# Kernel optimization log

Hardware: AMD Instinct MI355X
Metric: run time of the kernel (lower is better)

The kernel has to match this reference:

```python
import jax, jax.numpy as jnp
import numpy as np

HEADS = 4
HID = 64
EPS = 1e-5
SLOPE = 0.01  # torch default leaky_relu negative slope


def _lrelu(v):
    return jnp.where(v > 0, v, SLOPE * v)


def _gat_layer(x, e, att, num_nodes):
    # x: [N, H, d], e: [2, E], att: [1, H, 2d]
    d = x.shape[-1]
    att_l = att[0, :, :d]   # [H, d] multiplies src features
    att_r = att[0, :, d:]   # [H, d] multiplies dst features
    # mean over 2d of lrelu(cat(x[e0], x[e1]) * att) decomposes exactly into
    # per-node partial sums (leaky_relu is elementwise), avoiding the [E,H,2d] cat.
    s_l = _lrelu(x * att_l).sum(-1)  # [N, H]
    s_r = _lrelu(x * att_r).sum(-1)  # [N, H]
    s = jnp.exp((s_l[e[0]] + s_r[e[1]]) / (2 * d))  # [E, H]
    msg = x[e[1]] * s[..., None]                    # [E, H, d]
    num = jax.ops.segment_sum(msg, e[0], num_segments=num_nodes)  # [N, H, d]
    den = jax.ops.segment_sum(s, e[0], num_segments=num_nodes)    # [N, H]
    return num / den[..., None]


def _layernorm(h, gamma, beta):
    mu = h.mean(-1, keepdims=True)
    var = ((h - mu) ** 2).mean(-1, keepdims=True)
    return (h - mu) / jnp.sqrt(var + EPS) * gamma + beta


def setup_inputs() -> dict:
    key = jax.random.key(0)
    ks = jax.random.split(key, 10)
    N, DIN, E = 50000, 128, 800000
    H, D = HEADS, HID
    x = jax.random.normal(ks[0], (N, DIN), dtype=jnp.float32)
    edge_index = jax.random.randint(ks[1], (2, E), 0, N, dtype=jnp.int64)
    sc0 = 1.0 / np.sqrt(DIN)
    sc1 = 1.0 / np.sqrt(H * D)
    W0 = jax.random.uniform(ks[2], (H * D, DIN), jnp.float32, -sc0, sc0)
    b0 = jax.random.uniform(ks[3], (H * D,), jnp.float32, -sc0, sc0)
    W1 = jax.random.uniform(ks[4], (H * D, H * D), jnp.float32, -sc1, sc1)
    b1 = jax.random.uniform(ks[5], (H * D,), jnp.float32, -sc1, sc1)
    att0 = jax.random.uniform(ks[6], (1, H, 2 * D), jnp.float32)
    att1 = jax.random.uniform(ks[7], (1, H, 2 * D), jnp.float32)
    gamma = jnp.ones((H * D,), jnp.float32)
    beta = jnp.zeros((H * D,), jnp.float32)
    return {"x": x, "edge_index": edge_index, "W0": W0, "b0": b0,
            "W1": W1, "b1": b1, "att0": att0, "att1": att1,
            "gamma": gamma, "beta": beta}


def reference(x, edge_index, W0, b0, W1, b1, att0, att1, gamma, beta):
    N = x.shape[0]
    H, D = HEADS, HID
    e = edge_index
    # layer 0: gnn Linear -> attention aggregate -> LayerNorm + LeakyReLU
    h0 = (x @ W0.T + b0).reshape(N, H, D)
    a0 = _gat_layer(h0, e, att0, N).reshape(N, H * D)
    x1 = _lrelu(_layernorm(a0, gamma, beta))
    # layer 1 (last): attention aggregate then mean over heads, Identity act
    h1 = (x1 @ W1.T + b1).reshape(N, H, D)
    a1 = _gat_layer(h1, e, att1, N)  # [N, H, D]
    return a1.mean(axis=1)           # [N, D]
```

## Files before the change

kernel.cpp:

```cpp
#include <hip/hip_runtime.h>
#include <hip/hip_bf16.h>
#include <type_traits>

#define NN 50000
#define EE 800000
#define HH 4
#define DD 64
#define HD 256
#define DIN 128

typedef short bf16x8 __attribute__((ext_vector_type(8)));
typedef float f32x4 __attribute__((ext_vector_type(4)));

__device__ inline ushort f2bf(float x) {
    __hip_bfloat16 b = __float2bfloat16(x);
    return __builtin_bit_cast(ushort, b);
}
__device__ inline float bf2f(ushort u) {
    return __uint_as_float((uint)u << 16);
}

__device__ inline void gload16(const ushort* src, ushort* lds_dst) {
    __builtin_amdgcn_global_load_lds(
        (const __attribute__((address_space(1))) void*)src,
        (__attribute__((address_space(3))) void*)lds_dst, 16, 0, 0);
}


__global__ void hist_kernel(const int* __restrict__ e0, int* __restrict__ cnt, int E) {
    int i = blockIdx.x * 256 + threadIdx.x;
    if (i < E) atomicAdd(&cnt[e0[i]], 1);
}

__global__ __launch_bounds__(1024) void scanA_kernel(const int* __restrict__ cnt,
                                                     int* __restrict__ incl,
                                                     int* __restrict__ tot, int N) {
    __shared__ int buf[2][1024];
    int b = blockIdx.x, t = threadIdx.x;
    int i = b * 1024 + t;
    int v = (i < N) ? cnt[i] : 0;
    buf[0][t] = v;
    __syncthreads();
    int sel = 0;
    for (int off = 1; off < 1024; off <<= 1) {
        int nv = buf[sel][t];
        if (t >= off) nv += buf[sel][t - off];
        buf[sel ^ 1][t] = nv;
        __syncthreads();
        sel ^= 1;
    }
    if (i < N) incl[i] = buf[sel][t];
    if (t == 1023) tot[b] = buf[sel][1023];
}

__global__ void scanB_kernel(int* __restrict__ tot, int nb) {
    if (threadIdx.x == 0) {
        int s = 0;
        for (int b = 0; b < nb; ++b) {
            int v = tot[b];
            tot[b] = s;
            s += v;
        }
    }
}

__global__ void scanC_kernel(const int* __restrict__ incl, const int* __restrict__ tot,
                             const int* __restrict__ cnt, int* __restrict__ rp,
                             int* __restrict__ cur, int N) {
    int i = blockIdx.x * 256 + threadIdx.x;
    if (i == 0) rp[0] = 0;
    if (i < N) {
        int e = incl[i] + tot[i >> 10];
        rp[i + 1] = e;
        cur[i] = e - cnt[i];
    }
}

__global__ void scatter_kernel(const int* __restrict__ e0, const int* __restrict__ e1,
                               int* __restrict__ cur, int* __restrict__ col, int E) {
    int i = blockIdx.x * 256 + threadIdx.x;
    if (i < E) {
        int pos = atomicAdd(&cur[e0[i]], 1);
        col[pos] = e1[i];
    }
}


__global__ void split_kernel(const float* __restrict__ src, ushort* __restrict__ hi,
                             ushort* __restrict__ lo, int n4) {
    int i = blockIdx.x * 256 + threadIdx.x;
    if (i < n4) {
        float4 v = ((const float4*)src)[i];
        ushort4 h, l;
        h.x = f2bf(v.x); l.x = f2bf(v.x - bf2f(h.x));
        h.y = f2bf(v.y); l.y = f2bf(v.y - bf2f(h.y));
        h.z = f2bf(v.z); l.z = f2bf(v.z - bf2f(h.z));
        h.w = f2bf(v.w); l.w = f2bf(v.w - bf2f(h.w));
        ((ushort4*)hi)[i] = h;
        ((ushort4*)lo)[i] = l;
    }
}


template <int K>
__global__ __launch_bounds__(256) void gemm_mfma(const ushort* __restrict__ Ah,
                                                 const ushort* __restrict__ Al,
                                                 const ushort* __restrict__ Bh,
                                                 const ushort* __restrict__ Bl,
                                                 const float* __restrict__ bias,
                                                 const float* __restrict__ att,
                                                 ushort* __restrict__ Y,
                                                 float* __restrict__ bw,
                                                 int Nrows) {
    __shared__ ushort sh[2][20480];

    const int t = threadIdx.x;
    const int w = t >> 6, lane = t & 63;
    const int lg = lane >> 4;
    const int lm = lane & 15;
    const int row0 = blockIdx.x * 64;

    f32x4 acc[16];
#pragma unroll
    for (int n = 0; n < 16; ++n) acc[n] = (f32x4){0.f, 0.f, 0.f, 0.f};

    auto STAGE = [&](int b, int ks) {
        const int k0 = ks * 32;
        ushort* base = sh[b];
        gload16(Ah + (size_t)(row0 + lane) * K + k0 + w * 8, base + w * 512);
        gload16(Al + (size_t)(row0 + lane) * K + k0 + w * 8, base + 2048 + w * 512);
#pragma unroll
        for (int j2 = 0; j2 < 4; ++j2) {
            gload16(Bh + (size_t)(j2 * 64 + lane) * K + k0 + w * 8,
                    base + 4096 + w * 2048 + j2 * 512);
            gload16(Bl + (size_t)(j2 * 64 + lane) * K + k0 + w * 8,
                    base + 12288 + w * 2048 + j2 * 512);
        }
    };
    auto COMPUTE = [&](int b) {
        ushort* base = sh[b];
        bf16x8 ah = *(const bf16x8*)(base + lg * 512 + (w * 16 + lm) * 8);
        bf16x8 al = *(const bf16x8*)(base + 2048 + lg * 512 + (w * 16 + lm) * 8);
#pragma unroll
        for (int n = 0; n < 16; ++n) {
            bf16x8 bh = *(const bf16x8*)(base + 4096 + lg * 2048 + (n * 16 + lm) * 8);
            bf16x8 bl = *(const bf16x8*)(base + 12288 + lg * 2048 + (n * 16 + lm) * 8);
            acc[n] = __builtin_amdgcn_mfma_f32_16x16x32_bf16(ah, bh, acc[n], 0, 0, 0);
            acc[n] = __builtin_amdgcn_mfma_f32_16x16x32_bf16(ah, bl, acc[n], 0, 0, 0);
            acc[n] = __builtin_amdgcn_mfma_f32_16x16x32_bf16(al, bh, acc[n], 0, 0, 0);
        }
    };

    constexpr int NT = K / 32;
    STAGE(0, 0);
    asm volatile("s_waitcnt vmcnt(0)" ::: "memory");
    __syncthreads();
    int cur = 0;
#pragma unroll
    for (int ks = 0; ks < NT - 1; ++ks) {
        STAGE(cur ^ 1, ks + 1);
        COMPUTE(cur);
        asm volatile("s_waitcnt vmcnt(0)" ::: "memory");
        __syncthreads();
        cur ^= 1;
    }
    COMPUTE(cur);

    const int rbase = row0 + w * 16 + lg * 4;
    float attr[16];
#pragma unroll
    for (int n = 0; n < 16; ++n)
        attr[n] = att[(n >> 2) * 128 + 64 + (n & 3) * 16 + lm];
#pragma unroll
    for (int n = 0; n < 16; ++n) {
        const float bv = bias[n * 16 + lm];
        acc[n][0] += bv; acc[n][1] += bv; acc[n][2] += bv; acc[n][3] += bv;
    }
#pragma unroll
    for (int n = 0; n < 16; ++n) {
        const int c = n * 16 + lm;
#pragma unroll
        for (int r = 0; r < 4; ++r) {
            const int rr = rbase + r;
            if (rr < Nrows) Y[(size_t)rr * HD + c] = f2bf(acc[n][r]);
        }
    }
#pragma unroll
    for (int r = 0; r < 4; ++r) {
        float s0 = 0.f, s1 = 0.f, s2 = 0.f, s3 = 0.f;
#pragma unroll
        for (int n = 0; n < 16; ++n) {
            float p = acc[n][r] * attr[n];
            p = p > 0.f ? p : 0.01f * p;
            if ((n >> 2) == 0) s0 += p;
            else if ((n >> 2) == 1) s1 += p;
            else if ((n >> 2) == 2) s2 += p;
            else s3 += p;
        }
#pragma unroll
        for (int mm = 1; mm < 16; mm <<= 1) {
            s0 += __shfl_xor(s0, mm);
            s1 += __shfl_xor(s1, mm);
            s2 += __shfl_xor(s2, mm);
            s3 += __shfl_xor(s3, mm);
        }
        const int rr = rbase + r;
        if (lm < 4 && rr < Nrows) {
            float sv = lm == 0 ? s0 : lm == 1 ? s1 : lm == 2 ? s2 : s3;
            bw[rr * 4 + lm] = __expf(sv * 0.0078125f);
        }
    }
}


template <bool FINAL>
__global__ __launch_bounds__(256) void gather_kernel(const ushort* __restrict__ hbuf,
                                                     const int* __restrict__ rp,
                                                     const int* __restrict__ col,
                                                     const float* __restrict__ bw,
                                                     const float* __restrict__ gamma,
                                                     const float* __restrict__ beta,
                                                     float* __restrict__ out,
                                                     ushort* __restrict__ ohi,
                                                     ushort* __restrict__ olo) {
    const int t = threadIdx.x;
    const int w = t >> 6;
    const int lane = t & 63;
    const int hh = lane >> 4;
    const int n = blockIdx.x * 4 + w;

    __shared__ int cb[4][64];
    __shared__ float sv[4][256];

    const int start = rp[n], end = rp[n + 1];

    float acc0 = 0.f, acc1 = 0.f, acc2 = 0.f, acc3 = 0.f;
    float dn0 = 0.f, dn1 = 0.f, dn2 = 0.f, dn3 = 0.f;

    for (int base = start; base < end; base += 64) {
        int m = end - base;
        if (m > 64) m = 64;
        if (lane < m) {
            int src = col[base + lane];
            cb[w][lane] = src;
            float4 b4 = *(const float4*)(bw + src * 4);
            dn0 += b4.x; dn1 += b4.y; dn2 += b4.z; dn3 += b4.w;
            *(float4*)&sv[w][lane * 4] = b4;
        }
        __builtin_amdgcn_wave_barrier();
#pragma unroll 8
        for (int j = 0; j < m; ++j) {
            int src = cb[w][j];
            float s = sv[w][j * 4 + hh];
            ushort4 u = *(const ushort4*)(hbuf + (size_t)src * HD + lane * 4);
            acc0 = fmaf(bf2f(u.x), s, acc0);
            acc1 = fmaf(bf2f(u.y), s, acc1);
            acc2 = fmaf(bf2f(u.z), s, acc2);
            acc3 = fmaf(bf2f(u.w), s, acc3);
        }
        __builtin_amdgcn_wave_barrier();
    }

#pragma unroll
    for (int m2 = 32; m2 > 0; m2 >>= 1) {
        dn0 += __shfl_xor(dn0, m2);
        dn1 += __shfl_xor(dn1, m2);
        dn2 += __shfl_xor(dn2, m2);
        dn3 += __shfl_xor(dn3, m2);
    }
    float den = hh == 0 ? dn0 : hh == 1 ? dn1 : hh == 2 ? dn2 : dn3;
    float inv = 1.f / den;
    float r0 = acc0 * inv, r1 = acc1 * inv, r2 = acc2 * inv, r3 = acc3 * inv;

    if (!FINAL) {
        float s = r0 + r1 + r2 + r3;
#pragma unroll
        for (int m2 = 32; m2 > 0; m2 >>= 1) s += __shfl_xor(s, m2);
        float mu = s * (1.f / 256.f);
        float d0 = r0 - mu, d1 = r1 - mu, d2 = r2 - mu, d3 = r3 - mu;
        float vs = d0 * d0 + d1 * d1 + d2 * d2 + d3 * d3;
#pragma unroll
        for (int m2 = 32; m2 > 0; m2 >>= 1) vs += __shfl_xor(vs, m2);
        float rs = rsqrtf(vs * (1.f / 256.f) + 1e-5f);
        float4 g = *(const float4*)(gamma + lane * 4);
        float4 bb = *(const float4*)(beta + lane * 4);
        float y0 = d0 * rs * g.x + bb.x;
        float y1 = d1 * rs * g.y + bb.y;
        float y2 = d2 * rs * g.z + bb.z;
        float y3 = d3 * rs * g.w + bb.w;
        y0 = y0 > 0.f ? y0 : 0.01f * y0;
        y1 = y1 > 0.f ? y1 : 0.01f * y1;
        y2 = y2 > 0.f ? y2 : 0.01f * y2;
        y3 = y3 > 0.f ? y3 : 0.01f * y3;
        ushort4 h, l;
        h.x = f2bf(y0); l.x = f2bf(y0 - bf2f(h.x));
        h.y = f2bf(y1); l.y = f2bf(y1 - bf2f(h.y));
        h.z = f2bf(y2); l.z = f2bf(y2 - bf2f(h.z));
        h.w = f2bf(y3); l.w = f2bf(y3 - bf2f(h.w));
        *(ushort4*)(ohi + (size_t)n * HD + lane * 4) = h;
        *(ushort4*)(olo + (size_t)n * HD + lane * 4) = l;
    } else {
        r0 += __shfl_xor(r0, 16); r0 += __shfl_xor(r0, 32);
        r1 += __shfl_xor(r1, 16); r1 += __shfl_xor(r1, 32);
        r2 += __shfl_xor(r2, 16); r2 += __shfl_xor(r2, 32);
        r3 += __shfl_xor(r3, 16); r3 += __shfl_xor(r3, 32);
        if (lane < 16) {
            *(float4*)(out + (size_t)n * DD + lane * 4) =
                make_float4(r0 * 0.25f, r1 * 0.25f, r2 * 0.25f, r3 * 0.25f);
        }
    }
}


extern "C" void kernel_launch(void* const* d_in, const int* in_sizes, int n_in,
                              void* d_out, int out_size, void* d_ws, size_t ws_size,
                              hipStream_t stream) {
    const float* x     = (const float*)d_in[0];
    const int*   ei    = (const int*)d_in[1];
    const float* W0    = (const float*)d_in[2];
    const float* b0    = (const float*)d_in[3];
    const float* W1    = (const float*)d_in[4];
    const float* b1    = (const float*)d_in[5];
    const float* att0  = (const float*)d_in[6];
    const float* att1  = (const float*)d_in[7];
    const float* gamma = (const float*)d_in[8];
    const float* beta  = (const float*)d_in[9];
    float* out = (float*)d_out;

    const int N = NN, E = EE;

    ushort* ahi = (ushort*)d_ws;
    ushort* alo = ahi + (size_t)N * HD;
    ushort* hb0 = alo + (size_t)N * HD;
    ushort* hb1 = hb0 + (size_t)N * HD;
    ushort* xh  = hb1;
    ushort* xl  = hb1 + (size_t)N * DIN;
    ushort* w0h = hb1 + (size_t)N * HD;
    ushort* w0l = w0h + HD * DIN;
    ushort* w1h = w0l + HD * DIN;
    ushort* w1l = w1h + HD * HD;
    float* bw   = (float*)(w1l + HD * HD);
    int*   cnt  = (int*)(bw + (size_t)N * HH);
    int*   rp   = cnt + N;
    int*   cur  = rp + N + 1;
    int*   col  = cur + N;
    int*   incl = col + E;
    int*   tot  = incl + N;

    const int* e0 = ei;
    const int* e1 = ei + E;

    const int NB = (N + 1023) / 1024;

    hipMemsetAsync(cnt, 0, N * sizeof(int), stream);
    hist_kernel<<<(E + 255) / 256, 256, 0, stream>>>(e0, cnt, E);
    scanA_kernel<<<NB, 1024, 0, stream>>>(cnt, incl, tot, N);
    scanB_kernel<<<1, 64, 0, stream>>>(tot, NB);
    scanC_kernel<<<(N + 255) / 256, 256, 0, stream>>>(incl, tot, cnt, rp, cur, N);
    scatter_kernel<<<(E + 255) / 256, 256, 0, stream>>>(e0, e1, cur, col, E);

    split_kernel<<<(N * DIN / 4 + 255) / 256, 256, 0, stream>>>(x, xh, xl, N * DIN / 4);
    split_kernel<<<(HD * DIN / 4 + 255) / 256, 256, 0, stream>>>(W0, w0h, w0l, HD * DIN / 4);
    split_kernel<<<(HD * HD / 4 + 255) / 256, 256, 0, stream>>>(W1, w1h, w1l, HD * HD / 4);

    const int GB = (N + 63) / 64;

    gemm_mfma<DIN><<<GB, 256, 0, stream>>>(xh, xl, w0h, w0l, b0, att0, hb0, bw, N);
    gather_kernel<false><<<N / 4, 256, 0, stream>>>(hb0, rp, col, bw, gamma, beta,
                                                    nullptr, ahi, alo);

    gemm_mfma<HD><<<GB, 256, 0, stream>>>(ahi, alo, w1h, w1l, b1, att1, hb1, bw, N);
    gather_kernel<true><<<N / 4, 256, 0, stream>>>(hb1, rp, col, bw, gamma, beta,
                                                   out, nullptr, nullptr);
}
```

Measured before the change: 332.3 us.

## Retile GEMM warps over columns, overlap staging with compute, unroll gather loop

Each wave in the MFMA GEMM now owns a 64x64 tile (all 64 rows, one head's 64 columns) instead of 16 rows by 256 columns. This cuts per-step LDS fragment loads from 34 to 16 per wave and lets the attention-score reduction stay inside one wave per head. The pipeline now issues the next stage's loads, then waits with a partial vmcnt so the copy can overlap compute, and uses raw s_barrier instead of syncthreads. The gather inner loop unroll also rises from 8 to 16, which may raise register pressure.

After: 385.5 us. 1.16x slower.

```diff
diff --git a/kernel.cpp b/kernel.cpp
--- a/kernel.cpp
+++ b/kernel.cpp
@@ -120,9 +120,11 @@
     const int lm = lane & 15;
     const int row0 = blockIdx.x * 64;
 
-    f32x4 acc[16];
-#pragma unroll
-    for (int n = 0; n < 16; ++n) acc[n] = (f32x4){0.f, 0.f, 0.f, 0.f};
+    f32x4 acc[4][4];
+#pragma unroll
+    for (int rb = 0; rb < 4; ++rb)
+#pragma unroll
+        for (int cb = 0; cb < 4; ++cb) acc[rb][cb] = (f32x4){0.f, 0.f, 0.f, 0.f};
 
     auto STAGE = [&](int b, int ks) {
         const int k0 = ks * 32;
@@ -139,75 +141,86 @@
     };
     auto COMPUTE = [&](int b) {
         ushort* base = sh[b];
-        bf16x8 ah = *(const bf16x8*)(base + lg * 512 + (w * 16 + lm) * 8);
-        bf16x8 al = *(const bf16x8*)(base + 2048 + lg * 512 + (w * 16 + lm) * 8);
-#pragma unroll
-        for (int n = 0; n < 16; ++n) {
-            bf16x8 bh = *(const bf16x8*)(base + 4096 + lg * 2048 + (n * 16 + lm) * 8);
-            bf16x8 bl = *(const bf16x8*)(base + 12288 + lg * 2048 + (n * 16 + lm) * 8);
-            acc[n] = __builtin_amdgcn_mfma_f32_16x16x32_bf16(ah, bh, acc[n], 0, 0, 0);
-            acc[n] = __builtin_amdgcn_mfma_f32_16x16x32_bf16(ah, bl, acc[n], 0, 0, 0);
-            acc[n] = __builtin_amdgcn_mfma_f32_16x16x32_bf16(al, bh, acc[n], 0, 0, 0);
-        }
+        bf16x8 a_h[4], a_l[4], b_h[4], b_l[4];
+#pragma unroll
+        for (int rb = 0; rb < 4; ++rb) {
+            a_h[rb] = *(const bf16x8*)(base + lg * 512 + (rb * 16 + lm) * 8);
+            a_l[rb] = *(const bf16x8*)(base + 2048 + lg * 512 + (rb * 16 + lm) * 8);
+        }
+#pragma unroll
+        for (int cb = 0; cb < 4; ++cb) {
+            const int c = w * 64 + cb * 16 + lm;
+            b_h[cb] = *(const bf16x8*)(base + 4096 + lg * 2048 + c * 8);
+            b_l[cb] = *(const bf16x8*)(base + 12288 + lg * 2048 + c * 8);
+        }
+#pragma unroll
+        for (int rb = 0; rb < 4; ++rb)
+#pragma unroll
+            for (int cb = 0; cb < 4; ++cb) {
+                acc[rb][cb] = __builtin_amdgcn_mfma_f32_16x16x32_bf16(a_h[rb], b_h[cb],
+                                                                      acc[rb][cb], 0, 0, 0);
+                acc[rb][cb] = __builtin_amdgcn_mfma_f32_16x16x32_bf16(a_h[rb], b_l[cb],
+                                                                      acc[rb][cb], 0, 0, 0);
+                acc[rb][cb] = __builtin_amdgcn_mfma_f32_16x16x32_bf16(a_l[rb], b_h[cb],
+                                                                      acc[rb][cb], 0, 0, 0);
+            }
     };
 
     constexpr int NT = K / 32;
     STAGE(0, 0);
-    asm volatile("s_waitcnt vmcnt(0)" ::: "memory");
-    __syncthreads();
-    int cur = 0;
-#pragma unroll
-    for (int ks = 0; ks < NT - 1; ++ks) {
-        STAGE(cur ^ 1, ks + 1);
-        COMPUTE(cur);
-        asm volatile("s_waitcnt vmcnt(0)" ::: "memory");
-        __syncthreads();
-        cur ^= 1;
-    }
-    COMPUTE(cur);
-
-    const int rbase = row0 + w * 16 + lg * 4;
-    float attr[16];
-#pragma unroll
-    for (int n = 0; n < 16; ++n)
-        attr[n] = att[(n >> 2) * 128 + 64 + (n & 3) * 16 + lm];
-#pragma unroll
-    for (int n = 0; n < 16; ++n) {
-        const float bv = bias[n * 16 + lm];
-        acc[n][0] += bv; acc[n][1] += bv; acc[n][2] += bv; acc[n][3] += bv;
-    }
-#pragma unroll
-    for (int n = 0; n < 16; ++n) {
-        const int c = n * 16 + lm;
+#pragma unroll
+    for (int ks = 0; ks < NT; ++ks) {
+        const int cb_ = ks & 1;
+        if (ks + 1 < NT) {
+            STAGE(cb_ ^ 1, ks + 1);
+            asm volatile("s_waitcnt vmcnt(10)" ::: "memory");
+        } else {
+            asm volatile("s_waitcnt vmcnt(0)" ::: "memory");
+        }
+        __builtin_amdgcn_s_barrier();
+        COMPUTE(cb_);
+        __builtin_amdgcn_s_barrier();
+    }
+
+    float attr[4], bv[4];
+#pragma unroll
+    for (int cb = 0; cb < 4; ++cb) {
+        attr[cb] = att[w * 128 + 64 + cb * 16 + lm];
+        bv[cb] = bias[w * 64 + cb * 16 + lm];
+    }
+#pragma unroll
+    for (int rb = 0; rb < 4; ++rb)
+#pragma unroll
+        for (int cb = 0; cb < 4; ++cb) {
+            acc[rb][cb][0] += bv[cb]; acc[rb][cb][1] += bv[cb];
+            acc[rb][cb][2] += bv[cb]; acc[rb][cb][3] += bv[cb];
+        }
+#pragma unroll
+    for (int rb = 0; rb < 4; ++rb) {
+#pragma unroll
+        for (int cb = 0; cb < 4; ++cb) {
+            const int c = w * 64 + cb * 16 + lm;
+#pragma unroll
+            for (int r = 0; r < 4; ++r) {
+                const int rr = row0 + rb * 16 + lg * 4 + r;
+                if (rr < Nrows) Y[(size_t)rr * HD + c] = f2bf(acc[rb][cb][r]);
+            }
+        }
+    }
+#pragma unroll
+    for (int rb = 0; rb < 4; ++rb) {
 #pragma unroll
         for (int r = 0; r < 4; ++r) {
-            const int rr = rbase + r;
-            if (rr < Nrows) Y[(size_t)rr * HD + c] = f2bf(acc[n][r]);
-        }
-    }
-#pragma unroll
-    for (int r = 0; r < 4; ++r) {
-        float s0 = 0.f, s1 = 0.f, s2 = 0.f, s3 = 0.f;
-#pragma unroll
-        for (int n = 0; n < 16; ++n) {
-            float p = acc[n][r] * attr[n];
-            p = p > 0.f ? p : 0.01f * p;
-            if ((n >> 2) == 0) s0 += p;
-            else if ((n >> 2) == 1) s1 += p;
-            else if ((n >> 2) == 2) s2 += p;
-            else s3 += p;
-        }
-#pragma unroll
-        for (int mm = 1; mm < 16; mm <<= 1) {
-            s0 += __shfl_xor(s0, mm);
-            s1 += __shfl_xor(s1, mm);
-            s2 += __shfl_xor(s2, mm);
-            s3 += __shfl_xor(s3, mm);
-        }
-        const int rr = rbase + r;
-        if (lm < 4 && rr < Nrows) {
-            float sv = lm == 0 ? s0 : lm == 1 ? s1 : lm == 2 ? s2 : s3;
-            bw[rr * 4 + lm] = __expf(sv * 0.0078125f);
+            float s = 0.f;
+#pragma unroll
+            for (int cb = 0; cb < 4; ++cb) {
+                float p = acc[rb][cb][r] * attr[cb];
+                s += p > 0.f ? p : 0.01f * p;
+            }
+#pragma unroll
+            for (int mm = 1; mm < 16; mm <<= 1) s += __shfl_xor(s, mm);
+            const int rr = row0 + rb * 16 + lg * 4 + r;
+            if (lm == 0 && rr < Nrows) bw[rr * 4 + w] = __expf(s * 0.0078125f);
         }
     }
 }
@@ -248,7 +261,7 @@
             *(float4*)&sv[w][lane * 4] = b4;
         }
         __builtin_amdgcn_wave_barrier();
-#pragma unroll 8
+#pragma unroll 16
         for (int j = 0; j < m; ++j) {
             int src = cb[w][j];
             float s = sv[w][j * 4 + hh];
```
